# Optimization experiments

Measured on AMD Instinct MI355X. Metric: run time of the kernel, lower is better.

## Reference

```python
import jax, jax.numpy as jnp
import numpy as np

INPUT_SIZE = 128.0
CONF_THRESH = 0.75
IOU_THRESH = 0.3
MAX_DET = 100          # max_detections (top-k size)
SCORE_CLIP = 100.0
NUM_ANCHORS = 4194304


def setup_inputs() -> dict:
    key = jax.random.key(0)
    k1, k2, k3 = jax.random.split(key, 3)
    raw_boxes = jax.random.normal(k1, (1, NUM_ANCHORS, 16), dtype=jnp.float32)
    raw_scores = jax.random.normal(k2, (1, NUM_ANCHORS, 1), dtype=jnp.float32)
    anchors = jax.random.uniform(k3, (NUM_ANCHORS, 4), dtype=jnp.float32)  # [xc, yc, w, h] in [0,1]
    return {"raw_boxes": raw_boxes, "raw_scores": raw_scores, "anchors": anchors}


def _greedy_nms_keep(boxes_xyxy, iou_thresh):
    # boxes_xyxy: (K, 4) [x1, y1, x2, y2], sorted by descending score.
    # Returns bool keep mask, matching torchvision.ops.nms semantics
    # (suppress j if IoU(i, j) > thresh for some kept i < j).
    x1, y1, x2, y2 = boxes_xyxy[:, 0], boxes_xyxy[:, 1], boxes_xyxy[:, 2], boxes_xyxy[:, 3]
    area = (x2 - x1) * (y2 - y1)
    xx1 = jnp.maximum(x1[:, None], x1[None, :])
    yy1 = jnp.maximum(y1[:, None], y1[None, :])
    xx2 = jnp.minimum(x2[:, None], x2[None, :])
    yy2 = jnp.minimum(y2[:, None], y2[None, :])
    inter = jnp.clip(xx2 - xx1, 0.0) * jnp.clip(yy2 - yy1, 0.0)
    union = area[:, None] + area[None, :] - inter
    iou = inter / jnp.maximum(union, 1e-9)  # (K, K)
    K = boxes_xyxy.shape[0]
    later = jnp.arange(K)[None, :] > jnp.arange(K)[:, None]

    def body(i, keep):
        supp = (iou[i] > iou_thresh) & later[i] & keep[i]
        return keep & ~supp

    return jax.lax.fori_loop(0, K, body, jnp.ones((K,), dtype=bool))


def reference(raw_boxes, raw_scores, anchors):
    # Anchor decode (BlazeFace-style)
    xc = raw_boxes[..., 0] / INPUT_SIZE * anchors[:, 2] + anchors[:, 0]
    yc = raw_boxes[..., 1] / INPUT_SIZE * anchors[:, 3] + anchors[:, 1]
    w = raw_boxes[..., 2] / INPUT_SIZE * anchors[:, 2]
    h = raw_boxes[..., 3] / INPUT_SIZE * anchors[:, 3]
    ymin, xmin = yc - h * 0.5, xc - w * 0.5
    ymax, xmax = yc + h * 0.5, xc + w * 0.5
    # canonicalize (min/max reorder as in the torch code)
    boxes = jnp.stack([jnp.minimum(ymin, ymax), jnp.minimum(xmin, xmax),
                       jnp.maximum(ymin, ymax), jnp.maximum(xmin, xmax)], axis=-1)  # (B, A, 4)
    scores = jax.nn.sigmoid(jnp.clip(raw_scores, -SCORE_CLIP, SCORE_CLIP))[..., 0]  # (B, A)

    boxes0, scores0 = boxes[0], scores[0]
    topk_scores, topk_idx = jax.lax.top_k(scores0, MAX_DET)
    topk_boxes = boxes0[topk_idx]  # (K, 4) [ymin, xmin, ymax, xmax]

    boxes_xyxy = topk_boxes[:, jnp.array([1, 0, 3, 2])]  # -> [x1, y1, x2, y2]
    keep = _greedy_nms_keep(boxes_xyxy, IOU_THRESH)
    keep = keep & (topk_scores >= CONF_THRESH)

    # Fixed-shape output: suppressed/low-confidence rows zeroed (torch returns variable N)
    out_boxes = jnp.where(keep[:, None], topk_boxes, 0.0)
    out_scores = jnp.where(keep, topk_scores, 0.0)
    return jnp.concatenate([out_boxes, out_scores[:, None]], axis=-1)  # (K, 5)
```

## Files before the change

### kernel.cpp

```cpp
#include <hip/hip_runtime.h>
#include <math.h>

#define HBINS  4096
#define CAP    4096
#define MAXDET 100
#define NTHR   256
#define RAW_T0 3.5f

static __device__ __forceinline__ unsigned f2key(float f) {
    unsigned u = __float_as_uint(f);
    return (u & 0x80000000u) ? ~u : (u | 0x80000000u);
}

__global__ __launch_bounds__(NTHR) void k_compact_static(
    const float4* __restrict__ s4, int n4,
    unsigned* __restrict__ counter,
    float* __restrict__ cs, unsigned* __restrict__ ci) {
    int stride = gridDim.x * NTHR;
    for (int i = blockIdx.x * NTHR + threadIdx.x; i < n4; i += stride) {
        float4 v = s4[i];
        float f[4] = {v.x, v.y, v.z, v.w};
#pragma unroll
        for (int c = 0; c < 4; ++c) {
            if (f[c] > RAW_T0) {
                unsigned p = atomicAdd(counter, 1u);
                if (p < CAP) { cs[p] = f[c]; ci[p] = (unsigned)i * 4u + (unsigned)c; }
            }
        }
    }
}

__global__ __launch_bounds__(NTHR) void k_finalize(
    const float* __restrict__ rb, const float* __restrict__ an,
    const float4* __restrict__ s4, int n4,
    float* __restrict__ cs, unsigned* __restrict__ ci,
    const unsigned* __restrict__ counter,
    float* __restrict__ out) {
    __shared__ unsigned long long comp[CAP];
    __shared__ unsigned buf0[NTHR], buf1[NTHR];
    __shared__ unsigned s_tk, s_cnt;
    __shared__ float bx[MAXDET][4];
    __shared__ float ssc[MAXDET];
    __shared__ unsigned long long suppLo[MAXDET];
    __shared__ unsigned long long suppHi[MAXDET];
    __shared__ unsigned long long keepOut[2];

    int t = threadIdx.x;
    unsigned n = *counter;

    if (n < MAXDET || n > CAP) {
        unsigned* h = (unsigned*)comp;
        for (int i = t; i < HBINS; i += NTHR) h[i] = 0u;
        __syncthreads();
        for (int i = t; i < n4; i += NTHR) {
            float4 v = s4[i];
            atomicAdd(&h[f2key(v.x) >> 20], 1u);
            atomicAdd(&h[f2key(v.y) >> 20], 1u);
            atomicAdd(&h[f2key(v.z) >> 20], 1u);
            atomicAdd(&h[f2key(v.w) >> 20], 1u);
        }
        __syncthreads();
        unsigned loc[16];
        unsigned s = 0;
#pragma unroll
        for (int i = 0; i < 16; ++i) { loc[i] = h[t * 16 + i]; s += loc[i]; }
        buf0[t] = s;
        __syncthreads();
        unsigned* src = buf0; unsigned* dst = buf1;
        for (int off = 1; off < NTHR; off <<= 1) {
            unsigned v = src[t];
            if (t + off < NTHR) v += src[t + off];
            __syncthreads();
            dst[t] = v;
            __syncthreads();
            unsigned* tmp = src; src = dst; dst = tmp;
        }
        unsigned after = (t + 1 < NTHR) ? src[t + 1] : 0u;
        if (after < MAXDET && after + s >= MAXDET) {
            unsigned run = after;
#pragma unroll
            for (int i = 15; i >= 0; --i) {
                run += loc[i];
                if (run >= MAXDET) { s_tk = ((unsigned)(t * 16 + i)) << 20; break; }
            }
        }
        if (t == 0 && src[0] < MAXDET) s_tk = 0u;
        if (t == 0) s_cnt = 0u;
        __syncthreads();
        unsigned tk = s_tk;
        for (int i = t; i < n4; i += NTHR) {
            float4 v = s4[i];
            float f[4] = {v.x, v.y, v.z, v.w};
#pragma unroll
            for (int c = 0; c < 4; ++c) {
                if (f2key(f[c]) >= tk) {
                    unsigned p = atomicAdd(&s_cnt, 1u);
                    if (p < CAP) { cs[p] = f[c]; ci[p] = (unsigned)i * 4u + (unsigned)c; }
                }
            }
        }
        __syncthreads();
        n = s_cnt;
        if (n > CAP) n = CAP;
        __syncthreads();
    }

    for (unsigned i = (unsigned)t; i < n; i += NTHR) {
        comp[i] = ((unsigned long long)f2key(cs[i]) << 32) |
                  (unsigned long long)(0xFFFFFFFFu - ci[i]);
    }
    unsigned P = 128;
    while (P < n) P <<= 1;
    for (unsigned i = n + (unsigned)t; i < P; i += NTHR) comp[i] = 0ull;
    __syncthreads();

    for (unsigned k = 2; k <= P; k <<= 1) {
        for (unsigned j = k >> 1; j > 0; j >>= 1) {
            for (unsigned i = (unsigned)t; i < P; i += NTHR) {
                unsigned l = i ^ j;
                if (l > i) {
                    unsigned long long a = comp[i], b = comp[l];
                    bool up = ((i & k) == 0);
                    if (up ? (a < b) : (a > b)) { comp[i] = b; comp[l] = a; }
                }
            }
            __syncthreads();
        }
    }

    if (t < MAXDET) {
        unsigned long long gb = comp[t];
        float raw;
        unsigned id;
        if (gb == 0ull) {
            raw = -3.0e38f;
            id = 0u;
        } else {
            unsigned key = (unsigned)(gb >> 32);
            unsigned u = (key & 0x80000000u) ? (key & 0x7FFFFFFFu) : ~key;
            raw = __uint_as_float(u);
            id = 0xFFFFFFFFu - (unsigned)(gb & 0xFFFFFFFFull);
        }
        size_t b = (size_t)id * 16;
        float rb0 = rb[b + 0], rb1 = rb[b + 1], rb2 = rb[b + 2], rb3 = rb[b + 3];
        size_t a = (size_t)id * 4;
        float ax = an[a + 0], ay = an[a + 1], aw = an[a + 2], ah = an[a + 3];
        const float inv = 1.0f / 128.0f;
        float xc = rb0 * inv * aw + ax;
        float yc = rb1 * inv * ah + ay;
        float w  = rb2 * inv * aw;
        float h  = rb3 * inv * ah;
        float y0 = yc - h * 0.5f, y1 = yc + h * 0.5f;
        float x0 = xc - w * 0.5f, x1 = xc + w * 0.5f;
        bx[t][0] = fminf(y0, y1);
        bx[t][1] = fminf(x0, x1);
        bx[t][2] = fmaxf(y0, y1);
        bx[t][3] = fmaxf(x0, x1);
        float r = fminf(fmaxf(raw, -100.0f), 100.0f);
        ssc[t] = 1.0f / (1.0f + expf(-r));
        suppLo[t] = 0ull;
        suppHi[t] = 0ull;
    }
    __syncthreads();

    for (int p = t; p < MAXDET * MAXDET; p += NTHR) {
        int i = p / MAXDET, j = p - i * MAXDET;
        if (j > i) {
            float x1i = bx[i][1], y1i = bx[i][0], x2i = bx[i][3], y2i = bx[i][2];
            float x1j = bx[j][1], y1j = bx[j][0], x2j = bx[j][3], y2j = bx[j][2];
            float areai = (x2i - x1i) * (y2i - y1i);
            float areaj = (x2j - x1j) * (y2j - y1j);
            float xx1 = fmaxf(x1i, x1j), yy1 = fmaxf(y1i, y1j);
            float xx2 = fminf(x2i, x2j), yy2 = fminf(y2i, y2j);
            float iw = fmaxf(xx2 - xx1, 0.0f), ih = fmaxf(yy2 - yy1, 0.0f);
            float inter = iw * ih;
            float uni = areai + areaj - inter;
            float iou = inter / fmaxf(uni, 1e-9f);
            if (iou > 0.3f) {
                if (j < 64) atomicOr(&suppLo[i], 1ull << j);
                else        atomicOr(&suppHi[i], 1ull << (j - 64));
            }
        }
    }
    __syncthreads();

    if (t < 64) {
        unsigned long long a0 = suppLo[t], a1 = suppHi[t];
        unsigned long long b0 = (t < MAXDET - 64) ? suppLo[64 + t] : 0ull;
        unsigned long long b1 = (t < MAXDET - 64) ? suppHi[64 + t] : 0ull;
        unsigned long long kLo = ~0ull;
        unsigned long long kHi = (1ull << (MAXDET - 64)) - 1;
        for (int i = 0; i < MAXDET - 1; ++i) {
            bool kept = (i < 64) ? ((kLo >> i) & 1ull) : ((kHi >> (i - 64)) & 1ull);
            if (kept) {
                unsigned long long mLo = (i < 64) ? __shfl(a0, i) : __shfl(b0, i - 64);
                unsigned long long mHi = (i < 64) ? __shfl(a1, i) : __shfl(b1, i - 64);
                kLo &= ~mLo;
                kHi &= ~mHi;
            }
        }
        if (t == 0) { keepOut[0] = kLo; keepOut[1] = kHi; }
    }
    __syncthreads();

    if (t < MAXDET) {
        unsigned long long km = (t < 64) ? keepOut[0] : keepOut[1];
        bool kb = (km >> (t & 63)) & 1ull;
        bool k = kb && (ssc[t] >= 0.75f);
        float* o = out + t * 5;
        o[0] = k ? bx[t][0] : 0.0f;
        o[1] = k ? bx[t][1] : 0.0f;
        o[2] = k ? bx[t][2] : 0.0f;
        o[3] = k ? bx[t][3] : 0.0f;
        o[4] = k ? ssc[t]   : 0.0f;
    }
}

extern "C" void kernel_launch(void* const* d_in, const int* in_sizes, int n_in,
                              void* d_out, int out_size, void* d_ws, size_t ws_size,
                              hipStream_t stream) {
    const float* raw_boxes  = (const float*)d_in[0];
    const float* raw_scores = (const float*)d_in[1];
    const float* anchors    = (const float*)d_in[2];
    float* out = (float*)d_out;

    int n_scores = in_sizes[1];
    int n4 = n_scores / 4;

    unsigned* counter = (unsigned*)d_ws;
    float*    cs      = (float*)((char*)d_ws + 16);
    unsigned* ci      = (unsigned*)((char*)d_ws + 16400);

    hipMemsetAsync(counter, 0, 4, stream);

    k_compact_static<<<1024, NTHR, 0, stream>>>((const float4*)raw_scores, n4,
                                                counter, cs, ci);
    k_finalize<<<1, NTHR, 0, stream>>>(raw_boxes, anchors,
                                       (const float4*)raw_scores, n4,
                                       cs, ci, counter, out);
}
```

Measured before the change: 392.1 us.

## Compact candidates per block in shared memory and raise the prefilter threshold

The compaction kernel now buffers candidates in per-block shared memory, writing them as packed 64-bit keys plus a per-block count. This replaces the single global atomic counter and the memset that reset it. The finalize kernel prefix-scans the block counts to gather candidates, and falls back to the histogram path if any block overflows or the total is out of range. The raw-score threshold rises from 3.5 to 3.9, which shrinks the candidate set to sort, and box and anchor gathers use float4 loads. The risk is that the higher threshold sends more inputs into the slow full-scan fallback, for example when fewer than 100 candidates pass.

```diff
diff --git a/kernel.cpp b/kernel.cpp
--- a/kernel.cpp
+++ b/kernel.cpp
@@ -5,17 +5,29 @@
 #define CAP    4096
 #define MAXDET 100
 #define NTHR   256
-#define RAW_T0 3.5f
+#define NB     1024
+#define BPT    (NB / NTHR)
+#define BCAP   64
+#define RAW_T0 3.9f
 
 static __device__ __forceinline__ unsigned f2key(float f) {
     unsigned u = __float_as_uint(f);
     return (u & 0x80000000u) ? ~u : (u | 0x80000000u);
 }
 
-__global__ __launch_bounds__(NTHR) void k_compact_static(
+static __device__ __forceinline__ unsigned long long packcand(float s, unsigned idx) {
+    return ((unsigned long long)f2key(s) << 32) |
+           (unsigned long long)(0xFFFFFFFFu - idx);
+}
+
+__global__ __launch_bounds__(NTHR) void k_compact(
     const float4* __restrict__ s4, int n4,
-    unsigned* __restrict__ counter,
-    float* __restrict__ cs, unsigned* __restrict__ ci) {
+    unsigned* __restrict__ counts,
+    unsigned long long* __restrict__ cand) {
+    __shared__ unsigned lcnt;
+    __shared__ unsigned long long lbuf[BCAP];
+    if (threadIdx.x == 0) lcnt = 0u;
+    __syncthreads();
     int stride = gridDim.x * NTHR;
     for (int i = blockIdx.x * NTHR + threadIdx.x; i < n4; i += stride) {
         float4 v = s4[i];
@@ -23,22 +35,29 @@
 #pragma unroll
         for (int c = 0; c < 4; ++c) {
             if (f[c] > RAW_T0) {
-                unsigned p = atomicAdd(counter, 1u);
-                if (p < CAP) { cs[p] = f[c]; ci[p] = (unsigned)i * 4u + (unsigned)c; }
-            }
-        }
-    }
+                unsigned p = atomicAdd(&lcnt, 1u);
+                if (p < BCAP) lbuf[p] = packcand(f[c], (unsigned)(i * 4 + c));
+            }
+        }
+    }
+    __syncthreads();
+    unsigned c = lcnt;
+    unsigned m = c < BCAP ? c : BCAP;
+    for (unsigned j = threadIdx.x; j < m; j += NTHR)
+        cand[(size_t)blockIdx.x * BCAP + j] = lbuf[j];
+    if (threadIdx.x == 0) counts[blockIdx.x] = c;
 }
 
 __global__ __launch_bounds__(NTHR) void k_finalize(
     const float* __restrict__ rb, const float* __restrict__ an,
     const float4* __restrict__ s4, int n4,
-    float* __restrict__ cs, unsigned* __restrict__ ci,
-    const unsigned* __restrict__ counter,
+    const unsigned* __restrict__ counts,
+    const unsigned long long* __restrict__ cand,
     float* __restrict__ out) {
     __shared__ unsigned long long comp[CAP];
     __shared__ unsigned buf0[NTHR], buf1[NTHR];
     __shared__ unsigned s_tk, s_cnt;
+    __shared__ int s_bad;
     __shared__ float bx[MAXDET][4];
     __shared__ float ssc[MAXDET];
     __shared__ unsigned long long suppLo[MAXDET];
@@ -46,9 +65,47 @@
     __shared__ unsigned long long keepOut[2];
 
     int t = threadIdx.x;
-    unsigned n = *counter;
-
-    if (n < MAXDET || n > CAP) {
+    if (t == 0) s_bad = 0;
+    __syncthreads();
+
+    unsigned mycnt[BPT];
+    unsigned s = 0;
+#pragma unroll
+    for (int k = 0; k < BPT; ++k) {
+        unsigned c = counts[t * BPT + k];
+        if (c > BCAP) s_bad = 1;
+        mycnt[k] = c;
+        s += c;
+    }
+    buf0[t] = s;
+    __syncthreads();
+    unsigned* src = buf0; unsigned* dst = buf1;
+    for (int off = 1; off < NTHR; off <<= 1) {
+        unsigned v = src[t];
+        if (t >= off) v += src[t - off];
+        __syncthreads();
+        dst[t] = v;
+        __syncthreads();
+        unsigned* tmp = src; src = dst; dst = tmp;
+    }
+    unsigned total = src[NTHR - 1];
+    unsigned excl = src[t] - s;
+    __syncthreads();
+
+    bool fb = (total < MAXDET) || (total > CAP) || (s_bad != 0);
+    unsigned n;
+    if (!fb) {
+        unsigned off = excl;
+#pragma unroll
+        for (int k = 0; k < BPT; ++k) {
+            unsigned blk = (unsigned)(t * BPT + k);
+            unsigned c = mycnt[k];
+            for (unsigned j = 0; j < c; ++j)
+                comp[off + j] = cand[(size_t)blk * BCAP + j];
+            off += c;
+        }
+        n = total;
+    } else {
         unsigned* h = (unsigned*)comp;
         for (int i = t; i < HBINS; i += NTHR) h[i] = 0u;
         __syncthreads();
@@ -61,22 +118,22 @@
         }
         __syncthreads();
         unsigned loc[16];
-        unsigned s = 0;
-#pragma unroll
-        for (int i = 0; i < 16; ++i) { loc[i] = h[t * 16 + i]; s += loc[i]; }
-        buf0[t] = s;
-        __syncthreads();
-        unsigned* src = buf0; unsigned* dst = buf1;
+        unsigned ss = 0;
+#pragma unroll
+        for (int i = 0; i < 16; ++i) { loc[i] = h[t * 16 + i]; ss += loc[i]; }
+        buf0[t] = ss;
+        __syncthreads();
+        unsigned* fsrc = buf0; unsigned* fdst = buf1;
         for (int off = 1; off < NTHR; off <<= 1) {
-            unsigned v = src[t];
-            if (t + off < NTHR) v += src[t + off];
+            unsigned v = fsrc[t];
+            if (t + off < NTHR) v += fsrc[t + off];
             __syncthreads();
-            dst[t] = v;
+            fdst[t] = v;
             __syncthreads();
-            unsigned* tmp = src; src = dst; dst = tmp;
-        }
-        unsigned after = (t + 1 < NTHR) ? src[t + 1] : 0u;
-        if (after < MAXDET && after + s >= MAXDET) {
+            unsigned* tmp = fsrc; fsrc = fdst; fdst = tmp;
+        }
+        unsigned after = (t + 1 < NTHR) ? fsrc[t + 1] : 0u;
+        if (after < MAXDET && after + ss >= MAXDET) {
             unsigned run = after;
 #pragma unroll
             for (int i = 15; i >= 0; --i) {
@@ -84,7 +141,7 @@
                 if (run >= MAXDET) { s_tk = ((unsigned)(t * 16 + i)) << 20; break; }
             }
         }
-        if (t == 0 && src[0] < MAXDET) s_tk = 0u;
+        if (t == 0 && fsrc[0] < MAXDET) s_tk = 0u;
         if (t == 0) s_cnt = 0u;
         __syncthreads();
         unsigned tk = s_tk;
@@ -95,20 +152,15 @@
             for (int c = 0; c < 4; ++c) {
                 if (f2key(f[c]) >= tk) {
                     unsigned p = atomicAdd(&s_cnt, 1u);
-                    if (p < CAP) { cs[p] = f[c]; ci[p] = (unsigned)i * 4u + (unsigned)c; }
+                    if (p < CAP) comp[p] = packcand(f[c], (unsigned)(i * 4 + c));
                 }
             }
         }
         __syncthreads();
-        n = s_cnt;
-        if (n > CAP) n = CAP;
-        __syncthreads();
-    }
-
-    for (unsigned i = (unsigned)t; i < n; i += NTHR) {
-        comp[i] = ((unsigned long long)f2key(cs[i]) << 32) |
-                  (unsigned long long)(0xFFFFFFFFu - ci[i]);
-    }
+        n = s_cnt < CAP ? s_cnt : CAP;
+    }
+    __syncthreads();
+
     unsigned P = 128;
     while (P < n) P <<= 1;
     for (unsigned i = n + (unsigned)t; i < P; i += NTHR) comp[i] = 0ull;
@@ -141,15 +193,13 @@
             raw = __uint_as_float(u);
             id = 0xFFFFFFFFu - (unsigned)(gb & 0xFFFFFFFFull);
         }
-        size_t b = (size_t)id * 16;
-        float rb0 = rb[b + 0], rb1 = rb[b + 1], rb2 = rb[b + 2], rb3 = rb[b + 3];
-        size_t a = (size_t)id * 4;
-        float ax = an[a + 0], ay = an[a + 1], aw = an[a + 2], ah = an[a + 3];
+        float4 rbv = ((const float4*)rb)[(size_t)id * 4];
+        float4 av  = ((const float4*)an)[id];
         const float inv = 1.0f / 128.0f;
-        float xc = rb0 * inv * aw + ax;
-        float yc = rb1 * inv * ah + ay;
-        float w  = rb2 * inv * aw;
-        float h  = rb3 * inv * ah;
+        float xc = rbv.x * inv * av.z + av.x;
+        float yc = rbv.y * inv * av.w + av.y;
+        float w  = rbv.z * inv * av.z;
+        float h  = rbv.w * inv * av.w;
         float y0 = yc - h * 0.5f, y1 = yc + h * 0.5f;
         float x0 = xc - w * 0.5f, x1 = xc + w * 0.5f;
         bx[t][0] = fminf(y0, y1);
@@ -227,15 +277,11 @@
     int n_scores = in_sizes[1];
     int n4 = n_scores / 4;
 
-    unsigned* counter = (unsigned*)d_ws;
-    float*    cs      = (float*)((char*)d_ws + 16);
-    unsigned* ci      = (unsigned*)((char*)d_ws + 16400);
-
-    hipMemsetAsync(counter, 0, 4, stream);
-
-    k_compact_static<<<1024, NTHR, 0, stream>>>((const float4*)raw_scores, n4,
-                                                counter, cs, ci);
+    unsigned* counts          = (unsigned*)d_ws;
+    unsigned long long* cand  = (unsigned long long*)((char*)d_ws + 4096);
+
+    k_compact<<<NB, NTHR, 0, stream>>>((const float4*)raw_scores, n4, counts, cand);
     k_finalize<<<1, NTHR, 0, stream>>>(raw_boxes, anchors,
                                        (const float4*)raw_scores, n4,
-                                       cs, ci, counter, out);
-}
+                                       counts, cand, out);
+}
```

Measured after the change: 357.6 us. 1.1x faster.
